# Performance work log

Hardware: AMD Instinct MI355X
Metric: run time of the kernel (lower is better)

## Reference

```python
import jax, jax.numpy as jnp
import numpy as np
import itertools

B, T, C, H = 2, 2048, 1024, 8
HD = C // H  # head_dim = 128


def _head_dirs():
    # 8 trigrams = vertices of cube {-1,+1}^3, L2-normalized (norm sqrt(3))
    signs = [-1.0, 1.0]
    tri = np.array(list(itertools.product(signs, repeat=3)), dtype=np.float32)
    tri = tri / np.linalg.norm(tri, axis=1, keepdims=True)
    return jnp.asarray(tri[:H])  # [H, 3]


def setup_inputs() -> dict:
    key = jax.random.key(0)
    ks = jax.random.split(key, 5)
    w = lambda k, sh: jax.random.normal(k, sh, dtype=jnp.float32) * 0.02
    return {
        "x": jax.random.normal(ks[0], (B, T, C), dtype=jnp.float32),
        "Wq": w(ks[1], (H * 3, C)),
        "Wk": w(ks[2], (H * 3, C)),
        "Wv": w(ks[3], (C, C)),
        "Wo": w(ks[4], (C, C)),
        "scale": jnp.asarray(1.0 / np.sqrt(3.0), dtype=jnp.float32),
    }


def reference(x, Wq, Wk, Wv, Wo, scale):
    Bb, Tt, Cc = x.shape
    dirs = _head_dirs()  # [H, 3] constant buffer
    # tiny 3-dim per-head Q/K projections
    q3 = (x @ Wq.T).reshape(Bb, Tt, H, 3).transpose(0, 2, 1, 3)  # [B,H,T,3]
    k3 = (x @ Wk.T).reshape(Bb, Tt, H, 3).transpose(0, 2, 1, 3)  # [B,H,T,3]
    v = (x @ Wv.T).reshape(Bb, Tt, H, HD).transpose(0, 2, 1, 3)  # [B,H,T,HD]
    # projections of q/k onto each head's trigram direction
    q_on_dir = jnp.einsum('bhtd,hd->bht', q3, dirs)  # [B,H,T]
    k_on_dir = jnp.einsum('bhtd,hd->bht', k3, dirs)  # [B,H,T]
    # scores = scaled 3-dim dot product + geometric outer-product bias
    scores = jnp.einsum('bhtd,bhsd->bhts', q3, k3) * scale \
        + q_on_dir[..., :, None] * k_on_dir[..., None, :]  # [B,H,T,T]
    causal = jnp.tril(jnp.ones((Tt, Tt), dtype=bool))
    scores = jnp.where(causal, scores, -jnp.inf)
    attn = jax.nn.softmax(scores, axis=-1)
    out = jnp.einsum('bhts,bhsd->bhtd', attn, v)  # [B,H,T,HD]
    out = out.transpose(0, 2, 1, 3).reshape(Bb, Tt, Cc)
    return out @ Wo.T
```

## Files before the change

### kernel.cpp

```cpp
#include <hip/hip_runtime.h>
#include <hip/hip_bf16.h>

#define B_  2
#define T_  2048
#define C_  1024
#define H_  8
#define HD_ 128
#define M_  (B_*T_)

typedef short  bf16x8 __attribute__((ext_vector_type(8)));
typedef float  f32x4  __attribute__((ext_vector_type(4)));
typedef unsigned short u16x8 __attribute__((ext_vector_type(8)));

typedef const __attribute__((address_space(1))) void* gas_ptr;
typedef __attribute__((address_space(3))) void*       las_ptr;

#define L2E_ 1.4426950408889634f

static __device__ __forceinline__ unsigned short f2bf(float f) {
    unsigned int u = __float_as_uint(f);
    u += 0x7fffu + ((u >> 16) & 1u);
    return (unsigned short)(u >> 16);
}
static __device__ __forceinline__ float bf2f(unsigned short u) {
    return __uint_as_float(((unsigned int)u) << 16);
}
static __device__ __forceinline__ float exp2_fast(float x) {
#if __has_builtin(__builtin_amdgcn_exp2f)
    return __builtin_amdgcn_exp2f(x);
#else
    return exp2f(x);
#endif
}

__global__ __launch_bounds__(256) void k_convert_all(const float* __restrict__ x,
                                                     const float* __restrict__ Wv,
                                                     const float* __restrict__ Wo,
                                                     unsigned short* __restrict__ xbf,
                                                     unsigned short* __restrict__ wvbf,
                                                     unsigned short* __restrict__ wobf) {
    int i = blockIdx.x * 256 + threadIdx.x;
    const float* src; unsigned short* dst; int off;
    if (i < 1048576)      { src = x;  dst = xbf;  off = i; }
    else if (i < 1310720) { src = Wv; dst = wvbf; off = i - 1048576; }
    else                  { src = Wo; dst = wobf; off = i - 1310720; }
    float4 v = reinterpret_cast<const float4*>(src)[off];
    ushort4 o;
    o.x = f2bf(v.x); o.y = f2bf(v.y); o.z = f2bf(v.z); o.w = f2bf(v.w);
    reinterpret_cast<ushort4*>(dst)[off] = o;
}

__global__ __launch_bounds__(256) void k_proj_qk(const float* __restrict__ x,
                                                 const float* __restrict__ Wq,
                                                 const float* __restrict__ Wk,
                                                 const float* __restrict__ scale_p,
                                                 float* __restrict__ qt,
                                                 float* __restrict__ kt) {
    __shared__ __align__(16) float wl[48][260];
    __shared__ __align__(16) float xl[16][260];
    __shared__ float res[16][48];
    const int tid  = threadIdx.x;
    const int row0 = blockIdx.x << 4;
    const int r    = tid >> 4, sub = tid & 15;
    float a0 = 0.f, a1 = 0.f, a2 = 0.f;

    for (int ch = 0; ch < 4; ++ch) {
        const int k0 = ch * 256;
        #pragma unroll
        for (int i = 0; i < 12; ++i) {
            int fi = i * 256 + tid;
            int wr = fi >> 6, wc = (fi & 63) * 4;
            const float* src = (wr < 24) ? (Wq + (size_t)wr * C_) : (Wk + (size_t)(wr - 24) * C_);
            *reinterpret_cast<float4*>(&wl[wr][wc]) = *reinterpret_cast<const float4*>(src + k0 + wc);
        }
        #pragma unroll
        for (int i = 0; i < 4; ++i) {
            int fi = i * 256 + tid;
            int xr = fi >> 6, xc = (fi & 63) * 4;
            *reinterpret_cast<float4*>(&xl[xr][xc]) =
                *reinterpret_cast<const float4*>(x + (size_t)(row0 + xr) * C_ + k0 + xc);
        }
        __syncthreads();
        const int oc = sub * 3;
        #pragma unroll 4
        for (int k = 0; k < 256; k += 4) {
            float4 xv = *reinterpret_cast<const float4*>(&xl[r][k]);
            float4 w0 = *reinterpret_cast<const float4*>(&wl[oc + 0][k]);
            float4 w1 = *reinterpret_cast<const float4*>(&wl[oc + 1][k]);
            float4 w2 = *reinterpret_cast<const float4*>(&wl[oc + 2][k]);
            a0 += xv.x * w0.x + xv.y * w0.y + xv.z * w0.z + xv.w * w0.w;
            a1 += xv.x * w1.x + xv.y * w1.y + xv.z * w1.z + xv.w * w1.w;
            a2 += xv.x * w2.x + xv.y * w2.y + xv.z * w2.z + xv.w * w2.w;
        }
        __syncthreads();
    }
    res[r][sub * 3 + 0] = a0;
    res[r][sub * 3 + 1] = a1;
    res[r][sub * 3 + 2] = a2;
    __syncthreads();

    {
        const int rr = tid >> 4, s2 = tid & 15;
        const int isK = s2 >> 3, h = s2 & 7;
        const float r3 = 0.57735026918962576f;
        float d0 = (h & 4) ? r3 : -r3;
        float d1 = (h & 2) ? r3 : -r3;
        float d2 = (h & 1) ? r3 : -r3;
        const float* v3 = &res[rr][isK * 24 + h * 3];
        float a = v3[0], b = v3[1], c = v3[2];
        float ond = a * d0 + b * d1 + c * d2;
        float sc = scale_p[0];
        float4 ov = isK ? make_float4(a, b, c, ond)
                        : make_float4(a * sc * L2E_, b * sc * L2E_, c * sc * L2E_, ond * L2E_);
        float* dst = isK ? kt : qt;
        int grow = row0 + rr;
        int b_ = grow >> 11, t_idx = grow & (T_ - 1);
        reinterpret_cast<float4*>(dst)[(size_t)(b_ * H_ + h) * T_ + t_idx] = ov;
    }
}

template <int MODE>
__global__ __launch_bounds__(256) void k_gemm128x64(const unsigned short* __restrict__ A,
                                                    const unsigned short* __restrict__ Bw,
                                                    void* __restrict__ Cout,
                                                    int Mdim, int Ndim, int Kdim) {
    __shared__ __align__(16) unsigned short lds_a[4][128][8];
    __shared__ __align__(16) unsigned short lds_b[4][64][8];
    const int tid = threadIdx.x;
    const int nbn = Ndim >> 6;
    const int bm = (blockIdx.x / nbn) << 7;
    const int bn = (blockIdx.x % nbn) << 6;
    const int w = tid >> 6, l = tid & 63;
    const int wm = (w >> 1) << 6, wn = (w & 1) << 5;
    const int lh = l & 15, lq = l >> 4;

    f32x4 acc[4][2];
    #pragma unroll
    for (int i = 0; i < 4; ++i)
        #pragma unroll
        for (int j = 0; j < 2; ++j)
            acc[i][j] = (f32x4){0.f, 0.f, 0.f, 0.f};

    for (int k0 = 0; k0 < Kdim; k0 += 32) {
        #pragma unroll
        for (int p = 0; p < 2; ++p) {
            int flat = p * 256 + tid;
            int kq = flat >> 7, row = flat & 127;
            __builtin_amdgcn_global_load_lds((gas_ptr)(A + (size_t)(bm + row) * Kdim + k0 + kq * 8),
                (las_ptr)(&lds_a[0][0][0] + (size_t)flat * 8), 16, 0, 0);
        }
        {
            int kq = tid >> 6, row = tid & 63;
            __builtin_amdgcn_global_load_lds((gas_ptr)(Bw + (size_t)(bn + row) * Kdim + k0 + kq * 8),
                (las_ptr)(&lds_b[0][0][0] + (size_t)tid * 8), 16, 0, 0);
        }
        __syncthreads();

        bf16x8 af[4], bfr[2];
        #pragma unroll
        for (int f = 0; f < 4; ++f)
            af[f] = *reinterpret_cast<const bf16x8*>(&lds_a[lq][wm + f * 16 + lh][0]);
        #pragma unroll
        for (int f = 0; f < 2; ++f)
            bfr[f] = *reinterpret_cast<const bf16x8*>(&lds_b[lq][wn + f * 16 + lh][0]);
        #pragma unroll
        for (int i = 0; i < 4; ++i)
            #pragma unroll
            for (int j = 0; j < 2; ++j)
                acc[i][j] = __builtin_amdgcn_mfma_f32_16x16x32_bf16(af[i], bfr[j], acc[i][j], 0, 0, 0);
        __syncthreads();
    }

    if constexpr (MODE == 0) {
        float* Cf = (float*)Cout;
        #pragma unroll
        for (int i = 0; i < 4; ++i) {
            int rbase = bm + wm + i * 16 + lq * 4;
            #pragma unroll
            for (int j = 0; j < 2; ++j) {
                int cidx = bn + wn + j * 16 + lh;
                #pragma unroll
                for (int r = 0; r < 4; ++r)
                    Cf[(size_t)(rbase + r) * Ndim + cidx] = acc[i][j][r];
            }
        }
    } else {
        __shared__ unsigned short ldsT[128][72];
        #pragma unroll
        for (int i = 0; i < 4; ++i)
            #pragma unroll
            for (int j = 0; j < 2; ++j)
                #pragma unroll
                for (int r = 0; r < 4; ++r)
                    ldsT[wm + i * 16 + lq * 4 + r][wn + j * 16 + lh] = f2bf(acc[i][j][r]);
        __syncthreads();
        unsigned short* vt_out = (unsigned short*)Cout;
        int c = tid & 63, part = tid >> 6;
        int b = bm >> 11, t0 = bm & (T_ - 1);
        unsigned short* dst = vt_out + ((size_t)b * C_ + bn + c) * T_ + t0 + part * 32;
        #pragma unroll
        for (int jj = 0; jj < 4; ++jj) {
            u16x8 v;
            #pragma unroll
            for (int k = 0; k < 8; ++k) v[k] = ldsT[part * 32 + jj * 8 + k][c];
            *reinterpret_cast<u16x8*>(dst + jj * 8) = v;
        }
    }
}

__global__ __launch_bounds__(256) void k_attn_lds(
        const float4* __restrict__ qt, const float4* __restrict__ kt,
        const unsigned short* __restrict__ vt,
        unsigned short* __restrict__ mpart,
        float2* __restrict__ mlbuf,
        int nsp, int lg2nsp) {
    __shared__ __align__(16) unsigned short lv[2][4096];
    const int tid = threadIdx.x;
    const int w = tid >> 6, l = tid & 63;
    const int lh = l & 15, lg = l >> 4;
    const int bid = blockIdx.x;
    const int qb = 31 - (bid >> (4 + lg2nsp));
    const int sp = (bid >> 4) & (nsp - 1);
    const int bh = bid & 15;
    const int q0 = qb << 6;
    const int qrow = q0 + 4 * lh + w;
    const int nt = 2 * qb + 2;

    const float4* qtb = qt + (size_t)bh * T_;
    const float4* ktb = kt + (size_t)bh * T_;
    const unsigned short* vtb = vt + (size_t)bh * HD_ * T_;

    const int flatA = tid, flatB = 256 + tid;
    const unsigned short* srcA = vtb + (size_t)(((flatA >> 6) << 4) | (flatA & 15)) * T_ + ((flatA >> 4) & 3) * 8;
    const unsigned short* srcB = vtb + (size_t)(((flatB >> 6) << 4) | (flatB & 15)) * T_ + ((flatB >> 4) & 3) * 8;

#define STAGE_V(ST, BUF) do {                                                  \
    int s0e_ = (ST) << 5;                                                      \
    __builtin_amdgcn_global_load_lds((gas_ptr)(srcA + s0e_),                   \
        (las_ptr)(&lv[BUF][0] + (size_t)flatA * 8), 16, 0, 0);                 \
    __builtin_amdgcn_global_load_lds((gas_ptr)(srcB + s0e_),                   \
        (las_ptr)(&lv[BUF][0] + (size_t)flatB * 8), 16, 0, 0);                 \
} while (0)

    const float4 q4 = qtb[qrow];
    f32x4 acc[8];
    #pragma unroll
    for (int n = 0; n < 8; ++n) acc[n] = (f32x4){0.f, 0.f, 0.f, 0.f};
    float m = -1e30f, lsum = 0.f;

    if (sp < nt) STAGE_V(sp, 0);
    __syncthreads();

    int buf = 0;
    for (int st = sp; st < nt; st += nsp) {
        if (st + nsp < nt) STAGE_V(st + nsp, buf ^ 1);

        const int s0 = st << 5;
        const int sbase = s0 + lg * 8;

        float p[8];
        float mt = -1e30f;
        #pragma unroll
        for (int jj = 0; jj < 8; ++jj) {
            float4 k4 = ktb[sbase + jj];
            float sc = fmaf(q4.x, k4.x, fmaf(q4.y, k4.y, fmaf(q4.z, k4.z, q4.w * k4.w)));
            sc = (sbase + jj > qrow) ? -1e30f : sc;
            p[jj] = sc;
            mt = fmaxf(mt, sc);
        }
        mt = fmaxf(mt, __shfl_xor(mt, 16));
        mt = fmaxf(mt, __shfl_xor(mt, 32));
        if (__any(mt > m + 8.f)) {
            float mnew = fmaxf(m, mt);
            float corr = exp2_fast(m - mnew);
            m = mnew;
            lsum *= corr;
            float c0 = __shfl(corr, 4 * lg + 0);
            float c1 = __shfl(corr, 4 * lg + 1);
            float c2 = __shfl(corr, 4 * lg + 2);
            float c3 = __shfl(corr, 4 * lg + 3);
            #pragma unroll
            for (int n = 0; n < 8; ++n) {
                acc[n][0] *= c0; acc[n][1] *= c1; acc[n][2] *= c2; acc[n][3] *= c3;
            }
        }
        float ps = 0.f;
        #pragma unroll
        for (int jj = 0; jj < 8; ++jj) {
            float e = exp2_fast(p[jj] - m);
            e = (sbase + jj > qrow) ? 0.f : e;
            p[jj] = e;
            ps += e;
        }
        ps += __shfl_xor(ps, 16);
        ps += __shfl_xor(ps, 32);
        lsum += ps;

        bf16x8 pa;
        #pragma unroll
        for (int jj = 0; jj < 8; ++jj) pa[jj] = (short)f2bf(p[jj]);

        #pragma unroll
        for (int n = 0; n < 8; ++n) {
            bf16x8 vf = *reinterpret_cast<const bf16x8*>(&lv[buf][(size_t)(n * 64 + lg * 16 + lh) * 8]);
            acc[n] = __builtin_amdgcn_mfma_f32_16x16x32_bf16(pa, vf, acc[n], 0, 0, 0);
        }

        __syncthreads();
        buf ^= 1;
    }
#undef STAGE_V

    unsigned short* mp = mpart + (size_t)(sp * 16 + bh) * T_ * HD_;
    #pragma unroll
    for (int n = 0; n < 8; ++n) {
        #pragma unroll
        for (int r = 0; r < 4; ++r) {
            int row = q0 + 16 * lg + 4 * r + w;
            mp[(size_t)row * HD_ + n * 16 + lh] = f2bf(acc[n][r]);
        }
    }
    if (lg == 0)
        mlbuf[(size_t)(sp * 16 + bh) * T_ + qrow] = make_float2(m, lsum);
}

__global__ __launch_bounds__(256) void k_combine(const unsigned short* __restrict__ mpart,
                                                 const float2* __restrict__ mlbuf,
                                                 unsigned short* __restrict__ attnbf,
                                                 int nsp) {
    int idx = blockIdx.x * 256 + threadIdx.x;
    int bh = idx >> 16;
    int rem = idx & 65535;
    int t = rem >> 5, d0 = (rem & 31) * 4;
    float mg = -1e30f, den = 0.f;
    float ax = 0.f, ay = 0.f, az = 0.f, aw = 0.f;
    for (int s = 0; s < nsp; ++s) {
        float2 ml = mlbuf[(size_t)(s * 16 + bh) * T_ + t];
        ushort4 a = *reinterpret_cast<const ushort4*>(
            mpart + ((size_t)(s * 16 + bh) * T_ + t) * HD_ + d0);
        float mn = fmaxf(mg, ml.x);
        float cOld = exp2_fast(mg - mn);
        float cNew = exp2_fast(ml.x - mn);
        den = den * cOld + ml.y * cNew;
        ax = ax * cOld + bf2f(a.x) * cNew;
        ay = ay * cOld + bf2f(a.y) * cNew;
        az = az * cOld + bf2f(a.z) * cNew;
        aw = aw * cOld + bf2f(a.w) * cNew;
        mg = mn;
    }
    float inv = 1.f / den;
    int b = bh >> 3, h = bh & 7;
    ushort4 o;
    o.x = f2bf(ax * inv); o.y = f2bf(ay * inv);
    o.z = f2bf(az * inv); o.w = f2bf(aw * inv);
    *reinterpret_cast<ushort4*>(attnbf + ((size_t)(b * T_ + t) * C_ + h * HD_ + d0)) = o;
}

extern "C" void kernel_launch(void* const* d_in, const int* in_sizes, int n_in,
                              void* d_out, int out_size, void* d_ws, size_t ws_size,
                              hipStream_t stream) {
    const float* x     = (const float*)d_in[0];
    const float* Wq    = (const float*)d_in[1];
    const float* Wk    = (const float*)d_in[2];
    const float* Wv    = (const float*)d_in[3];
    const float* Wo    = (const float*)d_in[4];
    const float* scale = (const float*)d_in[5];
    float* out = (float*)d_out;

    const int nsp    = (ws_size >= 46137344) ? 4 : 2;
    const int lg2nsp = (nsp == 4) ? 2 : 1;

    char* ws = (char*)d_ws;
    size_t o = (size_t)nsp * 8388608;
    unsigned short* mpart  = (unsigned short*)(ws);
    unsigned short* xbf    = (unsigned short*)(ws);
    unsigned short* wvbf   = (unsigned short*)(ws + 8388608);
    float*          qt     = (float*)(ws + o);
    float*          kt     = (float*)(ws + o + 524288);
    unsigned short* vt     = (unsigned short*)(ws + o + 1048576);
    unsigned short* attnbf = (unsigned short*)(ws + o + 1048576);
    unsigned short* wobf   = (unsigned short*)(ws + o + 9437184);
    float2*         mlbuf  = (float2*)(ws + o + 11534336);

    k_convert_all<<<6144, 256, 0, stream>>>(x, Wv, Wo, xbf, wvbf, wobf);

    k_proj_qk<<<M_ / 16, 256, 0, stream>>>(x, Wq, Wk, scale, qt, kt);

    k_gemm128x64<2><<<(M_ / 128) * (C_ / 64), 256, 0, stream>>>(xbf, wvbf, (void*)vt, M_, C_, C_);

    k_attn_lds<<<32 * nsp * 16, 256, 0, stream>>>(
        reinterpret_cast<const float4*>(qt), reinterpret_cast<const float4*>(kt), vt,
        mpart, mlbuf, nsp, lg2nsp);

    k_combine<<<4096, 256, 0, stream>>>(mpart, mlbuf, attnbf, nsp);

    k_gemm128x64<0><<<(M_ / 128) * (C_ / 64), 256, 0, stream>>>(attnbf, wobf, (void*)out, M_, C_, C_);
}
```

Before: 150.3 us.

## Fuse x bf16 conversion into QK projection, deepen GEMM K-step, pair attention query blocks

The bf16 conversion of x now happens inside the Q/K projection kernel, which already reads x. This removes one full pass over x in the separate conversion kernel. The GEMM now stages 64 K-values per iteration instead of 32, halving the barrier count at the cost of twice the LDS. The attention kernel handles a short and a long causal query block per workgroup to balance work across workgroups, and it skips the causal mask outside diagonal tiles.

```diff
diff --git a/kernel.cpp b/kernel.cpp
--- a/kernel.cpp
+++ b/kernel.cpp
@@ -33,17 +33,14 @@
 #endif
 }
 
-__global__ __launch_bounds__(256) void k_convert_all(const float* __restrict__ x,
-                                                     const float* __restrict__ Wv,
-                                                     const float* __restrict__ Wo,
-                                                     unsigned short* __restrict__ xbf,
-                                                     unsigned short* __restrict__ wvbf,
-                                                     unsigned short* __restrict__ wobf) {
+__global__ __launch_bounds__(256) void k_convert_w(const float* __restrict__ Wv,
+                                                   const float* __restrict__ Wo,
+                                                   unsigned short* __restrict__ wvbf,
+                                                   unsigned short* __restrict__ wobf) {
     int i = blockIdx.x * 256 + threadIdx.x;
     const float* src; unsigned short* dst; int off;
-    if (i < 1048576)      { src = x;  dst = xbf;  off = i; }
-    else if (i < 1310720) { src = Wv; dst = wvbf; off = i - 1048576; }
-    else                  { src = Wo; dst = wobf; off = i - 1310720; }
+    if (i < 262144) { src = Wv; dst = wvbf; off = i; }
+    else            { src = Wo; dst = wobf; off = i - 262144; }
     float4 v = reinterpret_cast<const float4*>(src)[off];
     ushort4 o;
     o.x = f2bf(v.x); o.y = f2bf(v.y); o.z = f2bf(v.z); o.w = f2bf(v.w);
@@ -55,7 +52,8 @@
                                                  const float* __restrict__ Wk,
                                                  const float* __restrict__ scale_p,
                                                  float* __restrict__ qt,
-                                                 float* __restrict__ kt) {
+                                                 float* __restrict__ kt,
+                                                 unsigned short* __restrict__ xbf) {
     __shared__ __align__(16) float wl[48][260];
     __shared__ __align__(16) float xl[16][260];
     __shared__ float res[16][48];
@@ -77,8 +75,12 @@
         for (int i = 0; i < 4; ++i) {
             int fi = i * 256 + tid;
             int xr = fi >> 6, xc = (fi & 63) * 4;
-            *reinterpret_cast<float4*>(&xl[xr][xc]) =
-                *reinterpret_cast<const float4*>(x + (size_t)(row0 + xr) * C_ + k0 + xc);
+            size_t goff = (size_t)(row0 + xr) * C_ + k0 + xc;
+            float4 xv = *reinterpret_cast<const float4*>(x + goff);
+            *reinterpret_cast<float4*>(&xl[xr][xc]) = xv;
+            ushort4 o;
+            o.x = f2bf(xv.x); o.y = f2bf(xv.y); o.z = f2bf(xv.z); o.w = f2bf(xv.w);
+            *reinterpret_cast<ushort4*>(xbf + goff) = o;
         }
         __syncthreads();
         const int oc = sub * 3;
@@ -124,8 +126,8 @@
                                                     const unsigned short* __restrict__ Bw,
                                                     void* __restrict__ Cout,
                                                     int Mdim, int Ndim, int Kdim) {
-    __shared__ __align__(16) unsigned short lds_a[4][128][8];
-    __shared__ __align__(16) unsigned short lds_b[4][64][8];
+    __shared__ __align__(16) unsigned short lds_a[8][128][8];
+    __shared__ __align__(16) unsigned short lds_b[8][64][8];
     const int tid = threadIdx.x;
     const int nbn = Ndim >> 6;
     const int bm = (blockIdx.x / nbn) << 7;
@@ -141,33 +143,38 @@
         for (int j = 0; j < 2; ++j)
             acc[i][j] = (f32x4){0.f, 0.f, 0.f, 0.f};
 
-    for (int k0 = 0; k0 < Kdim; k0 += 32) {
-        #pragma unroll
-        for (int p = 0; p < 2; ++p) {
+    for (int k0 = 0; k0 < Kdim; k0 += 64) {
+        #pragma unroll
+        for (int p = 0; p < 4; ++p) {
             int flat = p * 256 + tid;
             int kq = flat >> 7, row = flat & 127;
             __builtin_amdgcn_global_load_lds((gas_ptr)(A + (size_t)(bm + row) * Kdim + k0 + kq * 8),
                 (las_ptr)(&lds_a[0][0][0] + (size_t)flat * 8), 16, 0, 0);
         }
-        {
-            int kq = tid >> 6, row = tid & 63;
+        #pragma unroll
+        for (int p = 0; p < 2; ++p) {
+            int flat = p * 256 + tid;
+            int kq = flat >> 6, row = flat & 63;
             __builtin_amdgcn_global_load_lds((gas_ptr)(Bw + (size_t)(bn + row) * Kdim + k0 + kq * 8),
-                (las_ptr)(&lds_b[0][0][0] + (size_t)tid * 8), 16, 0, 0);
-        }
-        __syncthreads();
-
-        bf16x8 af[4], bfr[2];
-        #pragma unroll
-        for (int f = 0; f < 4; ++f)
-            af[f] = *reinterpret_cast<const bf16x8*>(&lds_a[lq][wm + f * 16 + lh][0]);
-        #pragma unroll
-        for (int f = 0; f < 2; ++f)
-            bfr[f] = *reinterpret_cast<const bf16x8*>(&lds_b[lq][wn + f * 16 + lh][0]);
-        #pragma unroll
-        for (int i = 0; i < 4; ++i)
-            #pragma unroll
-            for (int j = 0; j < 2; ++j)
-                acc[i][j] = __builtin_amdgcn_mfma_f32_16x16x32_bf16(af[i], bfr[j], acc[i][j], 0, 0, 0);
+                (las_ptr)(&lds_b[0][0][0] + (size_t)flat * 8), 16, 0, 0);
+        }
+        __syncthreads();
+
+        #pragma unroll
+        for (int kk = 0; kk < 2; ++kk) {
+            bf16x8 af[4], bfr[2];
+            #pragma unroll
+            for (int f = 0; f < 4; ++f)
+                af[f] = *reinterpret_cast<const bf16x8*>(&lds_a[lq + 4 * kk][wm + f * 16 + lh][0]);
+            #pragma unroll
+            for (int f = 0; f < 2; ++f)
+                bfr[f] = *reinterpret_cast<const bf16x8*>(&lds_b[lq + 4 * kk][wn + f * 16 + lh][0]);
+            #pragma unroll
+            for (int i = 0; i < 4; ++i)
+                #pragma unroll
+                for (int j = 0; j < 2; ++j)
+                    acc[i][j] = __builtin_amdgcn_mfma_f32_16x16x32_bf16(af[i], bfr[j], acc[i][j], 0, 0, 0);
+        }
         __syncthreads();
     }
 
@@ -208,7 +215,7 @@
     }
 }
 
-__global__ __launch_bounds__(256) void k_attn_lds(
+__global__ __launch_bounds__(256) void k_attn_pair(
         const float4* __restrict__ qt, const float4* __restrict__ kt,
         const unsigned short* __restrict__ vt,
         unsigned short* __restrict__ mpart,
@@ -219,12 +226,9 @@
     const int w = tid >> 6, l = tid & 63;
     const int lh = l & 15, lg = l >> 4;
     const int bid = blockIdx.x;
-    const int qb = 31 - (bid >> (4 + lg2nsp));
+    const int qp = bid >> (4 + lg2nsp);
     const int sp = (bid >> 4) & (nsp - 1);
     const int bh = bid & 15;
-    const int q0 = qb << 6;
-    const int qrow = q0 + 4 * lh + w;
-    const int nt = 2 * qb + 2;
 
     const float4* qtb = qt + (size_t)bh * T_;
     const float4* ktb = kt + (size_t)bh * T_;
@@ -242,86 +246,114 @@
         (las_ptr)(&lv[BUF][0] + (size_t)flatB * 8), 16, 0, 0);                 \
 } while (0)
 
-    const float4 q4 = qtb[qrow];
-    f32x4 acc[8];
+    int buf = 0;
     #pragma unroll
-    for (int n = 0; n < 8; ++n) acc[n] = (f32x4){0.f, 0.f, 0.f, 0.f};
-    float m = -1e30f, lsum = 0.f;
-
-    if (sp < nt) STAGE_V(sp, 0);
-    __syncthreads();
-
-    int buf = 0;
-    for (int st = sp; st < nt; st += nsp) {
-        if (st + nsp < nt) STAGE_V(st + nsp, buf ^ 1);
-
-        const int s0 = st << 5;
-        const int sbase = s0 + lg * 8;
-
-        float p[8];
-        float mt = -1e30f;
-        #pragma unroll
-        for (int jj = 0; jj < 8; ++jj) {
-            float4 k4 = ktb[sbase + jj];
-            float sc = fmaf(q4.x, k4.x, fmaf(q4.y, k4.y, fmaf(q4.z, k4.z, q4.w * k4.w)));
-            sc = (sbase + jj > qrow) ? -1e30f : sc;
-            p[jj] = sc;
-            mt = fmaxf(mt, sc);
-        }
-        mt = fmaxf(mt, __shfl_xor(mt, 16));
-        mt = fmaxf(mt, __shfl_xor(mt, 32));
-        if (__any(mt > m + 8.f)) {
-            float mnew = fmaxf(m, mt);
-            float corr = exp2_fast(m - mnew);
-            m = mnew;
-            lsum *= corr;
-            float c0 = __shfl(corr, 4 * lg + 0);
-            float c1 = __shfl(corr, 4 * lg + 1);
-            float c2 = __shfl(corr, 4 * lg + 2);
-            float c3 = __shfl(corr, 4 * lg + 3);
+    for (int half = 0; half < 2; ++half) {
+        const int qb = half ? qp : (31 - qp);
+        const int q0 = qb << 6;
+        const int qrow = q0 + 4 * lh + w;
+        const int nt = 2 * qb + 2;
+
+        const float4 q4 = qtb[qrow];
+        f32x4 acc[8];
+        #pragma unroll
+        for (int n = 0; n < 8; ++n) acc[n] = (f32x4){0.f, 0.f, 0.f, 0.f};
+        float m = -1e30f, lsum = 0.f;
+
+        if (sp < nt) STAGE_V(sp, buf);
+        __syncthreads();
+
+        for (int st = sp; st < nt; st += nsp) {
+            if (st + nsp < nt) STAGE_V(st + nsp, buf ^ 1);
+
+            const int s0 = st << 5;
+            const int sbase = s0 + lg * 8;
+            const bool edge = (st >= 2 * qb);
+
+            float p[8];
+            float mt = -1e30f;
+            if (edge) {
+                #pragma unroll
+                for (int jj = 0; jj < 8; ++jj) {
+                    float4 k4 = ktb[sbase + jj];
+                    float sc = fmaf(q4.x, k4.x, fmaf(q4.y, k4.y, fmaf(q4.z, k4.z, q4.w * k4.w)));
+                    sc = (sbase + jj > qrow) ? -1e30f : sc;
+                    p[jj] = sc;
+                    mt = fmaxf(mt, sc);
+                }
+            } else {
+                #pragma unroll
+                for (int jj = 0; jj < 8; ++jj) {
+                    float4 k4 = ktb[sbase + jj];
+                    float sc = fmaf(q4.x, k4.x, fmaf(q4.y, k4.y, fmaf(q4.z, k4.z, q4.w * k4.w)));
+                    p[jj] = sc;
+                    mt = fmaxf(mt, sc);
+                }
+            }
+            mt = fmaxf(mt, __shfl_xor(mt, 16));
+            mt = fmaxf(mt, __shfl_xor(mt, 32));
+            if (__any(mt > m + 8.f)) {
+                float mnew = fmaxf(m, mt);
+                float corr = exp2_fast(m - mnew);
+                m = mnew;
+                lsum *= corr;
+                float c0 = __shfl(corr, 4 * lg + 0);
+                float c1 = __shfl(corr, 4 * lg + 1);
+                float c2 = __shfl(corr, 4 * lg + 2);
+                float c3 = __shfl(corr, 4 * lg + 3);
+                #pragma unroll
+                for (int n = 0; n < 8; ++n) {
+                    acc[n][0] *= c0; acc[n][1] *= c1; acc[n][2] *= c2; acc[n][3] *= c3;
+                }
+            }
+            float ps = 0.f;
+            if (edge) {
+                #pragma unroll
+                for (int jj = 0; jj < 8; ++jj) {
+                    float e = exp2_fast(p[jj] - m);
+                    e = (sbase + jj > qrow) ? 0.f : e;
+                    p[jj] = e;
+                    ps += e;
+                }
+            } else {
+                #pragma unroll
+                for (int jj = 0; jj < 8; ++jj) {
+                    float e = exp2_fast(p[jj] - m);
+                    p[jj] = e;
+                    ps += e;
+                }
+            }
+            ps += __shfl_xor(ps, 16);
+            ps += __shfl_xor(ps, 32);
+            lsum += ps;
+
+            bf16x8 pa;
+            #pragma unroll
+            for (int jj = 0; jj < 8; ++jj) pa[jj] = (short)f2bf(p[jj]);
+
             #pragma unroll
             for (int n = 0; n < 8; ++n) {
-                acc[n][0] *= c0; acc[n][1] *= c1; acc[n][2] *= c2; acc[n][3] *= c3;
-            }
-        }
-        float ps = 0.f;
-        #pragma unroll
-        for (int jj = 0; jj < 8; ++jj) {
-            float e = exp2_fast(p[jj] - m);
-            e = (sbase + jj > qrow) ? 0.f : e;
-            p[jj] = e;
-            ps += e;
-        }
-        ps += __shfl_xor(ps, 16);
-        ps += __shfl_xor(ps, 32);
-        lsum += ps;
-
-        bf16x8 pa;
-        #pragma unroll
-        for (int jj = 0; jj < 8; ++jj) pa[jj] = (short)f2bf(p[jj]);
-
+                bf16x8 vf = *reinterpret_cast<const bf16x8*>(&lv[buf][(size_t)(n * 64 + lg * 16 + lh) * 8]);
+                acc[n] = __builtin_amdgcn_mfma_f32_16x16x32_bf16(pa, vf, acc[n], 0, 0, 0);
+            }
+
+            __syncthreads();
+            buf ^= 1;
+        }
+
+        unsigned short* mp = mpart + (size_t)(sp * 16 + bh) * T_ * HD_;
         #pragma unroll
         for (int n = 0; n < 8; ++n) {
-            bf16x8 vf = *reinterpret_cast<const bf16x8*>(&lv[buf][(size_t)(n * 64 + lg * 16 + lh) * 8]);
-            acc[n] = __builtin_amdgcn_mfma_f32_16x16x32_bf16(pa, vf, acc[n], 0, 0, 0);
-        }
-
-        __syncthreads();
-        buf ^= 1;
+            #pragma unroll
+            for (int r = 0; r < 4; ++r) {
+                int row = q0 + 16 * lg + 4 * r + w;
+                mp[(size_t)row * HD_ + n * 16 + lh] = f2bf(acc[n][r]);
+            }
+        }
+        if (lg == 0)
+            mlbuf[(size_t)(sp * 16 + bh) * T_ + qrow] = make_float2(m, lsum);
     }
 #undef STAGE_V
-
-    unsigned short* mp = mpart + (size_t)(sp * 16 + bh) * T_ * HD_;
-    #pragma unroll
-    for (int n = 0; n < 8; ++n) {
-        #pragma unroll
-        for (int r = 0; r < 4; ++r) {
-            int row = q0 + 16 * lg + 4 * r + w;
-            mp[(size_t)row * HD_ + n * 16 + lh] = f2bf(acc[n][r]);
-        }
-    }
-    if (lg == 0)
-        mlbuf[(size_t)(sp * 16 + bh) * T_ + qrow] = make_float2(m, lsum);
 }
 
 __global__ __launch_bounds__(256) void k_combine(const unsigned short* __restrict__ mpart,
@@ -382,13 +414,13 @@
     unsigned short* wobf   = (unsigned short*)(ws + o + 9437184);
     float2*         mlbuf  = (float2*)(ws + o + 11534336);
 
-    k_convert_all<<<6144, 256, 0, stream>>>(x, Wv, Wo, xbf, wvbf, wobf);
-
-    k_proj_qk<<<M_ / 16, 256, 0, stream>>>(x, Wq, Wk, scale, qt, kt);
+    k_convert_w<<<2048, 256, 0, stream>>>(Wv, Wo, wvbf, wobf);
+
+    k_proj_qk<<<M_ / 16, 256, 0, stream>>>(x, Wq, Wk, scale, qt, kt, xbf);
 
     k_gemm128x64<2><<<(M_ / 128) * (C_ / 64), 256, 0, stream>>>(xbf, wvbf, (void*)vt, M_, C_, C_);
 
-    k_attn_lds<<<32 * nsp * 16, 256, 0, stream>>>(
+    k_attn_pair<<<16 * nsp * 16, 256, 0, stream>>>(
         reinterpret_cast<const float4*>(qt), reinterpret_cast<const float4*>(kt), vt,
         mpart, mlbuf, nsp, lg2nsp);
 
```

Result: slower. 156.3 us (+4.0%).
